# Kernel optimization log

Hardware: AMD Instinct MI355X
Metric: run time of the kernel (lower is better)

Reference implementation:

```python
import jax, jax.numpy as jnp
import numpy as np

EPS = 1e-10
TEMP = 1.0


def setup_inputs() -> dict:
    key = jax.random.key(0)
    ks = jax.random.split(key, 8)
    num_nodes, embed_dim, hidden_dim, num_edges = 50000, 128, 64, 600000
    node_embed = jax.random.normal(ks[0], (num_nodes, embed_dim), dtype=jnp.float32)
    edge_index = jax.random.randint(ks[1], (2, num_edges), 0, num_nodes, dtype=jnp.int64)
    u1 = jax.random.uniform(ks[2], (num_edges,), dtype=jnp.float32)
    u2 = jax.random.uniform(ks[3], (num_edges,), dtype=jnp.float32)
    # Linear weights (kaiming-ish scale)
    W1 = jax.random.normal(ks[4], (2 * embed_dim, hidden_dim), dtype=jnp.float32) * (1.0 / np.sqrt(2 * embed_dim))
    b1 = jnp.zeros((hidden_dim,), dtype=jnp.float32)
    W2 = jax.random.normal(ks[5], (hidden_dim, 1), dtype=jnp.float32) * (1.0 / np.sqrt(hidden_dim))
    b2 = jnp.zeros((1,), dtype=jnp.float32)
    return {"node_embed": node_embed, "edge_index": edge_index, "u1": u1, "u2": u2,
            "W1": W1, "b1": b1, "W2": W2, "b2": b2}


def reference(node_embed, edge_index, u1, u2, W1, b1, W2, b2):
    row, col = edge_index[0], edge_index[1]
    # gather + concat: [num_edges, 2*embed_dim]
    edge_feat = jnp.concatenate([node_embed[row], node_embed[col]], axis=1)
    # small MLP (dropout is identity in eval)
    h = jax.nn.relu(edge_feat @ W1 + b1)
    edge_logits = (h @ W2 + b2).squeeze(-1)  # [num_edges]
    # Gumbel-sigmoid (soft)
    g1 = -jnp.log(-jnp.log(jnp.clip(u1, EPS, 1.0 - EPS)))
    g2 = -jnp.log(-jnp.log(jnp.clip(u2, EPS, 1.0 - EPS)))
    edge_probs = jax.nn.sigmoid((edge_logits + g1 - g2) / TEMP)
    return edge_probs
```

## Files before the change

kernel.cpp:

```cpp
#include <hip/hip_runtime.h>
#include <stdint.h>

typedef float  floatx4 __attribute__((ext_vector_type(4)));
typedef short  short8  __attribute__((ext_vector_type(8)));
typedef float  f4v     __attribute__((ext_vector_type(4)));
typedef unsigned int uint32;

#define GS_EPS 1e-10f

__device__ __forceinline__ unsigned short f2bf(float x) {
  uint32 u = __float_as_uint(x);
  u += 0x7FFFu + ((u >> 16) & 1u);
  return (unsigned short)(u >> 16);
}
__device__ __forceinline__ float i8tof(uint32 w, int j) {
  int b = (int)(w << (24 - 8 * j)) >> 24;
  return (float)b;
}
__device__ __forceinline__ uint32 pack4_i8(floatx4 a, float inv) {
  uint32 r = 0;
#pragma unroll
  for (int i = 0; i < 4; ++i) {
    float x = a[i] * inv;
    x = fminf(fmaxf(x, -127.f), 127.f);
    int v = (int)__builtin_rintf(x);
    r |= ((uint32)(v & 255)) << (8 * i);
  }
  return r;
}

__global__ __launch_bounds__(512, 4) void pcompute_kernel(
    const float* __restrict__ E, const float* __restrict__ W1,
    const float* __restrict__ b1, uint8_t* __restrict__ P8,
    float2* __restrict__ Sc, int num_nodes) {
  __shared__ __align__(16) unsigned short w1blk[16 * 128 * 8];
  __shared__ float wmt[8], wmb[8];

  const int tid = threadIdx.x;
  const int wave = tid >> 6;
  const int lane = tid & 63;
  const int q = lane >> 4;
  const int l16 = lane & 15;

#pragma unroll
  for (int it = 0; it < 4; ++it) {
    int idx = it * 512 + tid;
    int chunk = idx >> 7;
    int n = idx & 127;
    const float* src = (n < 64) ? (W1 + n) : (W1 + 128 * 64 + (n - 64));
    uint32 d[4];
#pragma unroll
    for (int j = 0; j < 4; ++j) {
      int k0 = chunk * 8 + 2 * j;
      unsigned short lo = f2bf(src[(size_t)k0 * 64]);
      unsigned short hi = f2bf(src[(size_t)(k0 + 1) * 64]);
      d[j] = (uint32)lo | ((uint32)hi << 16);
    }
#pragma unroll
    for (int j = 0; j < 4; ++j) *(uint32*)&w1blk[(size_t)idx * 8 + 2 * j] = d[j];
  }

  const int rowbase = blockIdx.x * 128 + wave * 16;
  int row = rowbase + l16;
  const bool ok = row < num_nodes;
  if (!ok) row = num_nodes - 1;

  short8 bfr[4];
#pragma unroll
  for (int kk = 0; kk < 4; ++kk) {
    const float* p = E + (size_t)row * 128 + kk * 32 + q * 8;
    f4v v0 = *(const f4v*)p;
    f4v v1 = *(const f4v*)(p + 4);
    short8 t;
    t[0] = (short)f2bf(v0[0]); t[1] = (short)f2bf(v0[1]);
    t[2] = (short)f2bf(v0[2]); t[3] = (short)f2bf(v0[3]);
    t[4] = (short)f2bf(v1[0]); t[5] = (short)f2bf(v1[1]);
    t[6] = (short)f2bf(v1[2]); t[7] = (short)f2bf(v1[3]);
    bfr[kk] = t;
  }
  __syncthreads();

  floatx4 acc[8];
#pragma unroll
  for (int t = 0; t < 8; ++t) {
    floatx4 z = {0.f, 0.f, 0.f, 0.f};
    acc[t] = z;
  }
#pragma unroll
  for (int kk = 0; kk < 4; ++kk) {
#pragma unroll
    for (int t = 0; t < 8; ++t) {
      short8 af = *(const short8*)&w1blk[(size_t)((kk * 4 + q) * 128 + t * 16 + l16) * 8];
      acc[t] = __builtin_amdgcn_mfma_f32_16x16x32_bf16(af, bfr[kk], acc[t], 0, 0, 0);
    }
  }

  float mtop = 0.f, mbot = 0.f;
#pragma unroll
  for (int t = 0; t < 8; ++t) {
    floatx4 a = acc[t];
    if (t < 4) {
      f4v bv = *(const f4v*)(b1 + t * 16 + q * 4);
      a[0] += bv[0]; a[1] += bv[1]; a[2] += bv[2]; a[3] += bv[3];
      acc[t] = a;
    }
    float m = fmaxf(fmaxf(fabsf(a[0]), fabsf(a[1])), fmaxf(fabsf(a[2]), fabsf(a[3])));
    if (t < 4) mtop = fmaxf(mtop, m); else mbot = fmaxf(mbot, m);
  }
#pragma unroll
  for (int s = 1; s < 64; s <<= 1) {
    mtop = fmaxf(mtop, __shfl_xor(mtop, s, 64));
    mbot = fmaxf(mbot, __shfl_xor(mbot, s, 64));
  }
  if (lane == 0) {
    wmt[wave] = mtop;
    wmb[wave] = mbot;
  }
  __syncthreads();
  float bt = wmt[0], bb = wmb[0];
#pragma unroll
  for (int i = 1; i < 8; ++i) {
    bt = fmaxf(bt, wmt[i]);
    bb = fmaxf(bb, wmb[i]);
  }
  const float invt = 127.f / fmaxf(bt, 1e-20f);
  const float invb = 127.f / fmaxf(bb, 1e-20f);

  if (ok) {
    const int node = rowbase + l16;
#pragma unroll
    for (int t = 0; t < 8; ++t) {
      *(uint32*)(P8 + (size_t)node * 128 + t * 16 + q * 4) =
          pack4_i8(acc[t], (t < 4) ? invt : invb);
    }
  }
  if (tid == 0)
    Sc[blockIdx.x] = make_float2(bt * (1.f / 127.f), bb * (1.f / 127.f));
}

__global__ __launch_bounds__(256, 8) void edge_kernel(
    const uint8_t* __restrict__ P8, const float2* __restrict__ Sc,
    const int* __restrict__ ei,
    const float* __restrict__ u1, const float* __restrict__ u2,
    const float* __restrict__ W2, const float* __restrict__ b2,
    float* __restrict__ out, int num_edges, int nsc) {
  __shared__ float2 scs[2048];
  const int tid = threadIdx.x;
  const bool useLds = (nsc <= 2048);
  if (useLds) {
    for (int i = tid; i < nsc; i += 256) scs[i] = Sc[i];
  }

  const int wave = tid >> 6;
  const int lane = tid & 63;
  const int g = lane >> 2;
  const int h = lane & 3;
  const int wbase = blockIdx.x * 128 + wave * 32;

  f4v w0 = *(const f4v*)(W2 + h * 16);
  f4v w1v = *(const f4v*)(W2 + h * 16 + 4);
  f4v w2v = *(const f4v*)(W2 + h * 16 + 8);
  f4v w3v = *(const f4v*)(W2 + h * 16 + 12);
  const float bias2 = b2[0];

  int el = wbase + (lane & 31);
  if (el > num_edges - 1) el = num_edges - 1;
  unsigned long long oddmask = __ballot(ei[2 * el + 1] != 0);
  const bool idx64 = (oddmask == 0ULL);
  int eR, eC;
  if (idx64) {
    eR = ei[2 * el];
    eC = ei[2 * (num_edges + el)];
  } else {
    eR = ei[el];
    eC = ei[num_edges + el];
  }

  __syncthreads();

  uint4 ar[2], ac[2];
  float srv[2], scv[2];
#pragma unroll
  for (int s = 0; s < 2; ++s) {
    int nr = __shfl(eR, s * 16 + g, 64);
    int nc = __shfl(eC, s * 16 + g, 64);
    ar[s] = *(const uint4*)(P8 + (size_t)nr * 128 + h * 16);
    ac[s] = *(const uint4*)(P8 + (size_t)nc * 128 + 64 + h * 16);
    if (useLds) {
      srv[s] = scs[nr >> 7].x;
      scv[s] = scs[nc >> 7].y;
    } else {
      srv[s] = Sc[nr >> 7].x;
      scv[s] = Sc[nc >> 7].y;
    }
  }

#pragma unroll
  for (int s = 0; s < 2; ++s) {
    float accv = 0.f;
    const float st = srv[s], sb = scv[s];
    const uint32 rw[4] = {ar[s].x, ar[s].y, ar[s].z, ar[s].w};
    const uint32 cw[4] = {ac[s].x, ac[s].y, ac[s].z, ac[s].w};
    const f4v wv[4] = {w0, w1v, w2v, w3v};
#pragma unroll
    for (int wi = 0; wi < 4; ++wi) {
#pragma unroll
      for (int j = 0; j < 4; ++j) {
        float hv = fmaxf(i8tof(rw[wi], j) * st + i8tof(cw[wi], j) * sb, 0.f);
        accv = fmaf(hv, wv[wi][j], accv);
      }
    }
    accv += __shfl_xor(accv, 1, 64);
    accv += __shfl_xor(accv, 2, 64);
    if (h == 0) {
      int e = wbase + s * 16 + g;
      if (e < num_edges) {
        float a1 = fminf(fmaxf(u1[e], GS_EPS), 1.0f);
        float a2 = fminf(fmaxf(u2[e], GS_EPS), 1.0f);
        float g1 = -__logf(-__logf(a1));
        float g2 = -__logf(-__logf(a2));
        float x = accv + bias2 + g1 - g2;
        out[e] = 1.f / (1.f + __expf(-x));
      }
    }
  }
}

extern "C" void kernel_launch(void* const* d_in, const int* in_sizes, int n_in,
                              void* d_out, int out_size, void* d_ws, size_t ws_size,
                              hipStream_t stream) {
  const float* node_embed = (const float*)d_in[0];
  const int* ei = (const int*)d_in[1];
  const float* u1 = (const float*)d_in[2];
  const float* u2 = (const float*)d_in[3];
  const float* W1 = (const float*)d_in[4];
  const float* b1 = (const float*)d_in[5];
  const float* W2 = (const float*)d_in[6];
  const float* b2 = (const float*)d_in[7];
  float* out = (float*)d_out;

  const int num_edges = in_sizes[2];
  const int num_nodes = in_sizes[0] / 128;
  const int pblocks = (num_nodes + 127) / 128;

  char* w = (char*)d_ws;
  uint8_t* P8 = (uint8_t*)w;   w += ((size_t)num_nodes * 128 + 255) & ~(size_t)255;
  float2* Sc = (float2*)w;

  pcompute_kernel<<<pblocks, 512, 0, stream>>>(node_embed, W1, b1, P8, Sc, num_nodes);
  const int eblocks = (num_edges + 127) / 128;
  edge_kernel<<<eblocks, 256, 0, stream>>>(P8, Sc, ei, u1, u2, W2, b2, out, num_edges, pblocks);
}
```

Measured before the change: 110.7 us.

## Fuse node projection and edge scoring into one cooperative persistent kernel

Replaces the two-kernel sequence with a single cooperative kernel. It first quantizes node projections over 64-row tiles in a grid-stride loop, then runs a grid-wide sync, then scores edges in a grid-stride loop. Per-tile scales are staged in LDS by reusing the W1 buffer. The aim is to remove the launch gap between the kernels. The costs are a grid barrier, repeated W1 conversion in every persistent block, and smaller quantization tiles. If the cooperative launch fails, it falls back to the old two kernels.

```diff
diff --git a/kernel.cpp b/kernel.cpp
--- a/kernel.cpp
+++ b/kernel.cpp
@@ -1,5 +1,8 @@
 #include <hip/hip_runtime.h>
+#include <hip/hip_cooperative_groups.h>
 #include <stdint.h>
+
+namespace cg = cooperative_groups;
 
 typedef float  floatx4 __attribute__((ext_vector_type(4)));
 typedef short  short8  __attribute__((ext_vector_type(8)));
@@ -27,6 +30,192 @@
     r |= ((uint32)(v & 255)) << (8 * i);
   }
   return r;
+}
+
+__global__ __launch_bounds__(256, 4) void fused_kernel(
+    const float* __restrict__ E, const float* __restrict__ W1,
+    const float* __restrict__ b1, const int* __restrict__ ei,
+    const float* __restrict__ u1, const float* __restrict__ u2,
+    const float* __restrict__ W2, const float* __restrict__ b2,
+    uint8_t* __restrict__ P8, float2* __restrict__ Sc,
+    float* __restrict__ out, int num_nodes, int num_edges, int ntiles) {
+  __shared__ __align__(16) unsigned short w1blk[16 * 128 * 8];
+  __shared__ float wmt[4], wmb[4];
+
+  const int tid = threadIdx.x;
+  const int wave = tid >> 6;
+  const int lane = tid & 63;
+  const int q = lane >> 4;
+  const int l16 = lane & 15;
+
+#pragma unroll
+  for (int it = 0; it < 8; ++it) {
+    int idx = it * 256 + tid;
+    int chunk = idx >> 7;
+    int n = idx & 127;
+    const float* src = (n < 64) ? (W1 + n) : (W1 + 128 * 64 + (n - 64));
+    uint32 d[4];
+#pragma unroll
+    for (int j = 0; j < 4; ++j) {
+      int k0 = chunk * 8 + 2 * j;
+      unsigned short lo = f2bf(src[(size_t)k0 * 64]);
+      unsigned short hi = f2bf(src[(size_t)(k0 + 1) * 64]);
+      d[j] = (uint32)lo | ((uint32)hi << 16);
+    }
+#pragma unroll
+    for (int j = 0; j < 4; ++j) *(uint32*)&w1blk[(size_t)idx * 8 + 2 * j] = d[j];
+  }
+  __syncthreads();
+
+  for (int t0 = blockIdx.x; t0 < ntiles; t0 += gridDim.x) {
+    const int rowbase = t0 * 64 + wave * 16;
+    int row = rowbase + l16;
+    const bool ok = row < num_nodes;
+    if (!ok) row = num_nodes - 1;
+
+    short8 bfr[4];
+#pragma unroll
+    for (int kk = 0; kk < 4; ++kk) {
+      const float* p = E + (size_t)row * 128 + kk * 32 + q * 8;
+      f4v v0 = *(const f4v*)p;
+      f4v v1 = *(const f4v*)(p + 4);
+      short8 t;
+      t[0] = (short)f2bf(v0[0]); t[1] = (short)f2bf(v0[1]);
+      t[2] = (short)f2bf(v0[2]); t[3] = (short)f2bf(v0[3]);
+      t[4] = (short)f2bf(v1[0]); t[5] = (short)f2bf(v1[1]);
+      t[6] = (short)f2bf(v1[2]); t[7] = (short)f2bf(v1[3]);
+      bfr[kk] = t;
+    }
+
+    floatx4 acc[8];
+#pragma unroll
+    for (int t = 0; t < 8; ++t) {
+      floatx4 z = {0.f, 0.f, 0.f, 0.f};
+      acc[t] = z;
+    }
+#pragma unroll
+    for (int kk = 0; kk < 4; ++kk) {
+#pragma unroll
+      for (int t = 0; t < 8; ++t) {
+        short8 af = *(const short8*)&w1blk[(size_t)((kk * 4 + q) * 128 + t * 16 + l16) * 8];
+        acc[t] = __builtin_amdgcn_mfma_f32_16x16x32_bf16(af, bfr[kk], acc[t], 0, 0, 0);
+      }
+    }
+
+    float mtop = 0.f, mbot = 0.f;
+#pragma unroll
+    for (int t = 0; t < 8; ++t) {
+      floatx4 a = acc[t];
+      if (t < 4) {
+        f4v bv = *(const f4v*)(b1 + t * 16 + q * 4);
+        a[0] += bv[0]; a[1] += bv[1]; a[2] += bv[2]; a[3] += bv[3];
+        acc[t] = a;
+      }
+      float m = fmaxf(fmaxf(fabsf(a[0]), fabsf(a[1])), fmaxf(fabsf(a[2]), fabsf(a[3])));
+      if (t < 4) mtop = fmaxf(mtop, m); else mbot = fmaxf(mbot, m);
+    }
+#pragma unroll
+    for (int s = 1; s < 64; s <<= 1) {
+      mtop = fmaxf(mtop, __shfl_xor(mtop, s, 64));
+      mbot = fmaxf(mbot, __shfl_xor(mbot, s, 64));
+    }
+    if (lane == 0) {
+      wmt[wave] = mtop;
+      wmb[wave] = mbot;
+    }
+    __syncthreads();
+    float bt = fmaxf(fmaxf(wmt[0], wmt[1]), fmaxf(wmt[2], wmt[3]));
+    float bb = fmaxf(fmaxf(wmb[0], wmb[1]), fmaxf(wmb[2], wmb[3]));
+    const float invt = 127.f / fmaxf(bt, 1e-20f);
+    const float invb = 127.f / fmaxf(bb, 1e-20f);
+
+    if (ok) {
+      const int node = rowbase + l16;
+#pragma unroll
+      for (int t = 0; t < 8; ++t) {
+        *(uint32*)(P8 + (size_t)node * 128 + t * 16 + q * 4) =
+            pack4_i8(acc[t], (t < 4) ? invt : invb);
+      }
+    }
+    if (tid == 0)
+      Sc[t0] = make_float2(bt * (1.f / 127.f), bb * (1.f / 127.f));
+    __syncthreads();
+  }
+
+  __threadfence();
+  cg::this_grid().sync();
+
+  float2* scs = (float2*)w1blk;
+  for (int i = tid; i < ntiles; i += 256) scs[i] = Sc[i];
+  __syncthreads();
+
+  const int g = lane >> 2;
+  const int h = lane & 3;
+  f4v w0 = *(const f4v*)(W2 + h * 16);
+  f4v w1v = *(const f4v*)(W2 + h * 16 + 4);
+  f4v w2v = *(const f4v*)(W2 + h * 16 + 8);
+  f4v w3v = *(const f4v*)(W2 + h * 16 + 12);
+  const float bias2 = b2[0];
+
+  for (int base = blockIdx.x * 128; base < num_edges; base += gridDim.x * 128) {
+    const int wbase = base + wave * 32;
+    if (wbase >= num_edges) continue;
+
+    int el = wbase + (lane & 31);
+    if (el > num_edges - 1) el = num_edges - 1;
+    unsigned long long oddmask = __ballot(ei[2 * el + 1] != 0);
+    const bool idx64 = (oddmask == 0ULL);
+    int eR, eC;
+    if (idx64) {
+      eR = ei[2 * el];
+      eC = ei[2 * (num_edges + el)];
+    } else {
+      eR = ei[el];
+      eC = ei[num_edges + el];
+    }
+
+    uint4 ar[2], ac[2];
+    float srv[2], scv[2];
+#pragma unroll
+    for (int s = 0; s < 2; ++s) {
+      int nr = __shfl(eR, s * 16 + g, 64);
+      int nc = __shfl(eC, s * 16 + g, 64);
+      ar[s] = *(const uint4*)(P8 + (size_t)nr * 128 + h * 16);
+      ac[s] = *(const uint4*)(P8 + (size_t)nc * 128 + 64 + h * 16);
+      srv[s] = scs[nr >> 6].x;
+      scv[s] = scs[nc >> 6].y;
+    }
+
+#pragma unroll
+    for (int s = 0; s < 2; ++s) {
+      float accv = 0.f;
+      const float st = srv[s], sb = scv[s];
+      const uint32 rw[4] = {ar[s].x, ar[s].y, ar[s].z, ar[s].w};
+      const uint32 cw[4] = {ac[s].x, ac[s].y, ac[s].z, ac[s].w};
+      const f4v wv[4] = {w0, w1v, w2v, w3v};
+#pragma unroll
+      for (int wi = 0; wi < 4; ++wi) {
+#pragma unroll
+        for (int j = 0; j < 4; ++j) {
+          float hv = fmaxf(i8tof(rw[wi], j) * st + i8tof(cw[wi], j) * sb, 0.f);
+          accv = fmaf(hv, wv[wi][j], accv);
+        }
+      }
+      accv += __shfl_xor(accv, 1, 64);
+      accv += __shfl_xor(accv, 2, 64);
+      if (h == 0) {
+        int e = wbase + s * 16 + g;
+        if (e < num_edges) {
+          float a1 = fminf(fmaxf(u1[e], GS_EPS), 1.0f);
+          float a2 = fminf(fmaxf(u2[e], GS_EPS), 1.0f);
+          float g1 = -__logf(-__logf(a1));
+          float g2 = -__logf(-__logf(a2));
+          float x = accv + bias2 + g1 - g2;
+          out[e] = 1.f / (1.f + __expf(-x));
+        }
+      }
+    }
+  }
 }
 
 __global__ __launch_bounds__(512, 4) void pcompute_kernel(
@@ -241,13 +430,29 @@
 
   const int num_edges = in_sizes[2];
   const int num_nodes = in_sizes[0] / 128;
-  const int pblocks = (num_nodes + 127) / 128;
+  const int ntiles = (num_nodes + 63) / 64;
 
   char* w = (char*)d_ws;
   uint8_t* P8 = (uint8_t*)w;   w += ((size_t)num_nodes * 128 + 255) & ~(size_t)255;
   float2* Sc = (float2*)w;
 
-  pcompute_kernel<<<pblocks, 512, 0, stream>>>(node_embed, W1, b1, P8, Sc, num_nodes);
-  const int eblocks = (num_edges + 127) / 128;
-  edge_kernel<<<eblocks, 256, 0, stream>>>(P8, Sc, ei, u1, u2, W2, b2, out, num_edges, pblocks);
-}
+  int maxb = 0;
+  hipOccupancyMaxActiveBlocksPerMultiprocessor(&maxb, fused_kernel, 256, 0);
+  if (maxb < 1) maxb = 1;
+  long long grid = (long long)maxb * 256;
+  if (grid > 1024) grid = 1024;
+
+  void* args[] = {(void*)&node_embed, (void*)&W1, (void*)&b1, (void*)&ei,
+                  (void*)&u1, (void*)&u2, (void*)&W2, (void*)&b2,
+                  (void*)&P8, (void*)&Sc, (void*)&out,
+                  (void*)&num_nodes, (void*)&num_edges, (void*)&ntiles};
+  hipError_t err = hipLaunchCooperativeKernel(
+      fused_kernel, dim3((uint32_t)grid), dim3(256), args, 0, stream);
+
+  if (err != hipSuccess) {
+    const int pblocks = (num_nodes + 127) / 128;
+    pcompute_kernel<<<pblocks, 512, 0, stream>>>(node_embed, W1, b1, P8, Sc, num_nodes);
+    const int eblocks = (num_edges + 127) / 128;
+    edge_kernel<<<eblocks, 256, 0, stream>>>(P8, Sc, ei, u1, u2, W2, b2, out, num_edges, pblocks);
+  }
+}
```

Result: slower. 226.5 us (+104.6%).
